# Optimization experiments

Hardware: AMD Instinct MI355X
Metric: run time of the kernel (lower is better)

Reference implementation:

```python
import jax, jax.numpy as jnp
import numpy as np

N_HIDDEN = 512
BATCH = 16
MAX_LEN = 4096


def setup_inputs() -> dict:
    key = jax.random.key(0)
    k1, k2, k3 = jax.random.split(key, 3)
    h = jax.random.normal(k1, (BATCH, N_HIDDEN, MAX_LEN), dtype=jnp.float32)
    # Conv1d weight [out_ch=3*nh, in_ch=nh, kernel=2], fan-in scaled
    W = jax.random.normal(k2, (3 * N_HIDDEN, N_HIDDEN, 2), dtype=jnp.float32) / np.float32(np.sqrt(2.0 * N_HIDDEN))
    b = 0.02 * jax.random.normal(k3, (3 * N_HIDDEN,), dtype=jnp.float32)
    b = b.at[2 * N_HIDDEN:].set(1.0)  # init_gate_bias on the gate third of the bias
    # lengths: grouped (unique_consecutive) and sorted descending, padded into width MAX_LEN
    N = jnp.array([4096] * 4 + [3000] * 4 + [2048] * 4 + [1000] * 4, dtype=jnp.int32)
    return {"h": h, "W": W, "b": b, "N": N}


def _conv_reduce(h, W, b):
    # _reduce: Conv1d(nh -> 3*nh, kernel=2, stride=2) then gated combine (dropout=0).
    B, C, L = h.shape
    Lp = L + (L % 2)
    x = jnp.pad(h, ((0, 0), (0, 0), (0, Lp - L))).reshape(B, C, Lp // 2, 2)
    lrg = jnp.einsum('bclk,ock->bol', x, W) + b[None, :, None]  # [B, 3C, L//2]
    l = lrg[:, :C]
    r = jnp.tanh(lrg[:, C:2 * C])
    g = jax.nn.sigmoid(lrg[:, 2 * C:])
    return l * g + r * (1.0 - g)


def _forward(h, W, b, N):
    B, nh, L = h.shape
    # Nfp2 = largest power of two <= N ; M = 2*(N - Nfp2)
    Nfp2 = (2 ** jnp.floor(jnp.log2(N.astype(jnp.float32)))).astype(N.dtype)
    M = 2 * (N - Nfp2)
    # --- prefix reduce + suffix cat (padded/masked equivalent of _suffix_cat) ---
    # conv is local (k=2, s=2), so reducing the full padded width gives identical
    # values at the kept positions j < M//2.
    red = _conv_reduce(h, W, b)                      # [B, nh, ceil(L/2)]
    red = jnp.pad(red, ((0, 0), (0, 0), (0, L - red.shape[-1])))
    j = jnp.arange(L)
    half = (M // 2)[:, None]                         # [B, 1]
    take_red = j[None, :] < half                     # first M//2 slots <- reduced prefix
    idx = jnp.where(take_red, j[None, :], jnp.minimum(j[None, :] + half, L - 1))
    suf = jnp.take_along_axis(h, jnp.broadcast_to(idx[:, None, :], (B, nh, L)), axis=2)
    cur = jnp.where(take_red[:, None, :], red, suf)  # per-seq length now Nfp2 (power of 2)
    n = Nfp2
    # --- halving tree reduction; freeze sequences that reached length 1 ---
    steps = int(np.floor(np.log2(L)))
    for _ in range(steps):
        red = _conv_reduce(cur, W, b)
        neww = red.shape[-1]
        active = (n > 1)[:, None, None]
        cur = jnp.where(active, red, cur[:, :, :neww])
        n = jnp.where(n > 1, n // 2, n)
    return cur[:, :, 0]  # squeeze(-1) -> [B, nh]


def reference(h, W, b, N):
    return _forward(h, W, b, N)
```

## Files before the change

kernel.cpp:

```cpp
#include <hip/hip_runtime.h>

#define BATCH 16
#define CH 512
#define OC 1536
#define KDIM 1024
#define LMAX 4096
#define WGLOB_SZ 3145728

typedef __attribute__((ext_vector_type(8))) _Float16 h8v;
typedef __attribute__((ext_vector_type(4))) float f4v;

__device__ __forceinline__ int nfp2_of(int n) { return 1 << (31 - __clz(n)); }

__device__ __forceinline__ unsigned short h2u(_Float16 h) {
  union { _Float16 h; unsigned short u; } v; v.h = h; return v.u;
}

__device__ __forceinline__ void layout(const int* __restrict__ Nvec, int b,
                                       size_t& offC0, size_t& offA, size_t& offB,
                                       int& n, int& nfp2, int& half) {
  size_t c0t = 0, at = 0, bt = 0, c0o = 0, ao = 0, bo = 0;
  n = 2; nfp2 = 2; half = 0;
#pragma unroll 1
  for (int i = 0; i < BATCH; ++i) {
    int ni = Nvec[i];
    int f = nfp2_of(ni);
    int hf = ni - f;
    size_t cs = (size_t)((hf + 127) & ~127) << 11;
    size_t as = (size_t)(f >> 1) << 11;
    size_t bs = (size_t)(f >> 2) << 11;
    if (i < b) { c0o += cs; ao += as; bo += bs; }
    if (i == b) { n = ni; nfp2 = f; half = hf; }
    c0t += cs; at += as; bt += bs;
  }
  offC0 = (size_t)WGLOB_SZ + c0o;
  offA = (size_t)WGLOB_SZ + c0t + ao;
  offB = (size_t)WGLOB_SZ + c0t + at + bo;
}

__device__ __forceinline__ void gload16(const void* g, void* l) {
  __builtin_amdgcn_global_load_lds((const __attribute__((address_space(1))) void*)g,
                                   (__attribute__((address_space(3))) void*)l, 16, 0, 0);
}

__global__ __launch_bounds__(256) void prep_w_k(const float* __restrict__ W, char* __restrict__ ws) {
  int idx = blockIdx.x * 256 + threadIdx.x;
  if (idx >= 16 * 1536) return;
  int step = idx / 1536;
  int o = idx - step * 1536;
  const float* src = W + (size_t)o * KDIM + step * 64;
  unsigned short hb[64];
#pragma unroll
  for (int t = 0; t < 64; ++t) hb[t] = h2u((_Float16)src[t]);
  uint4* d4 = (uint4*)(ws + ((size_t)idx << 7));
#pragma unroll
  for (int s = 0; s < 8; ++s) {
    int oc = (s ^ (o & 7)) * 8;
    uint4 v;
    v.x = (unsigned)hb[oc + 0] | ((unsigned)hb[oc + 1] << 16);
    v.y = (unsigned)hb[oc + 2] | ((unsigned)hb[oc + 3] << 16);
    v.z = (unsigned)hb[oc + 4] | ((unsigned)hb[oc + 5] << 16);
    v.w = (unsigned)hb[oc + 6] | ((unsigned)hb[oc + 7] << 16);
    d4[s] = v;
  }
}

__global__ __launch_bounds__(256) void reorg_h_k(const float* __restrict__ h,
                                                 const int* __restrict__ Nvec,
                                                 char* __restrict__ ws,
                                                 float* __restrict__ dout, int mode) {
  __shared__ char T[32 * 256];
  const int b = blockIdx.z;
  size_t offC0, offA, offB; int n, nfp2, half;
  layout(Nvec, b, offC0, offA, offB, n, nfp2, half);
  const int tid = threadIdx.x;
  const int by = blockIdx.y;
  const int c0 = by * 64;

  if (mode == 1 && nfp2 == 1) {
    if (blockIdx.x == 0 && tid < 64)
      dout[(size_t)b * CH + c0 + tid] = h[(size_t)b * CH * LMAX + (size_t)(c0 + tid) * LMAX];
    return;
  }

  const int d0 = blockIdx.x * 32;
  int dlo, dhi, soff;
  size_t base;
  if (mode == 0) { dlo = 0; dhi = half; soff = 0; base = offC0; }
  else { dlo = half >> 1; dhi = nfp2 >> 1; soff = half; base = offA; }
  if (d0 >= dhi || d0 + 32 <= dlo) return;

  const float* hb = h + (size_t)b * CH * LMAX;

#pragma unroll
  for (int q = 0; q < 8; ++q) {
    int id = q * 256 + tid;
    int cl = id >> 5;
    int dl = id & 31;
    int d = d0 + dl;
    bool ok = (d < dhi) && (d >= dlo);
    float2 v;
    v.x = 0.f; v.y = 0.f;
    if (ok) v = *(const float2*)(hb + (size_t)(c0 + cl) * LMAX + 2 * d + soff);
    unsigned u = (unsigned)h2u((_Float16)v.x) | ((unsigned)h2u((_Float16)v.y) << 16);
    int g = cl >> 2;
    *(unsigned*)(T + dl * 256 + ((g ^ (dl & 15)) << 4) + (cl & 3) * 4) = u;
  }
  __syncthreads();
#pragma unroll
  for (int qq = 0; qq < 2; ++qq) {
    int gid = qq * 256 + tid;
    int dl = gid >> 4;
    int s = gid & 15;
    int d = d0 + dl;
    if (d >= dhi || d < dlo) continue;
    uint4 val = *(const uint4*)(T + dl * 256 + ((s ^ (dl & 15)) << 4));
    size_t dst = base + ((size_t)d << 11) + (size_t)((2 * by + (s >> 3)) << 7) +
                 (((s & 7) ^ (d & 7)) << 4);
    *(uint4*)(ws + dst) = val;
  }
}

__global__ __launch_bounds__(256, 2) void mfma_level_k(const float* __restrict__ bias,
                                                       const int* __restrict__ Nvec,
                                                       char* __restrict__ ws,
                                                       float* __restrict__ dout,
                                                       int level, int tiles) {
  __shared__ char smem[81920];
  const int id = blockIdx.x;
  const int o0 = (id & 7) * 64;
  const int r2 = id >> 3;
  const int xb = r2 % tiles;
  const int b = r2 / tiles;
  if (b >= BATCH) return;

  size_t offC0, offA, offB; int n, nfp2, half;
  layout(Nvec, b, offC0, offA, offB, n, nfp2, half);

  int cols;
  size_t inOff, outOff;
  if (level == 0) {
    if (half == 0) return;
    cols = half;
    inOff = offC0;
    outOff = offA;
  } else {
    int w = nfp2 >> (level - 1);
    if (w < 2) return;
    cols = w >> 1;
    inOff = (level & 1) ? offA : offB;
    outOff = (level & 1) ? offB : offA;
  }
  const bool fin = (level > 0) && ((nfp2 >> level) == 1);
  const int l0 = xb * 128;
  if (l0 >= cols) return;

  const int tid = threadIdx.x;
  const int lane = tid & 63, wid = tid >> 6;
  const int lane15 = lane & 15, lq = lane >> 4;
  const int rg = wid & 1, cg = wid >> 1;
  const char* inp = ws + inOff;

  unsigned aoff[6]; int adst[6];
#pragma unroll
  for (int q = 0; q < 6; ++q) {
    int d = q * 4096 + tid * 16;
    int r = d >> 7;
    int p = d & 127;
    int o = ((r >> 6) << 9) + o0 + (r & 63);
    aoff[q] = ((unsigned)o << 7) + p;
    adst[q] = q * 4096 + wid * 1024;
  }
  unsigned boff[4]; int bdst[4];
#pragma unroll
  for (int q = 0; q < 4; ++q) {
    int d = q * 4096 + tid * 16;
    int l = d >> 7;
    int p = d & 127;
    int lc = l0 + l; if (lc > cols - 1) lc = cols - 1;
    boff[q] = ((unsigned)lc << 11) + p;
    bdst[q] = q * 4096 + wid * 1024;
  }

#define STAGE(st, sel) do {                                                  \
    char* Ab = smem + (sel) * 24576;                                         \
    char* Bb = smem + 49152 + (sel) * 16384;                                 \
    unsigned ka = (unsigned)(st) * 196608u;                                  \
    unsigned kb = (unsigned)(st) << 7;                                       \
    _Pragma("unroll") for (int q = 0; q < 6; ++q)                            \
      gload16(ws + ka + aoff[q], Ab + adst[q]);                              \
    _Pragma("unroll") for (int q = 0; q < 4; ++q)                            \
      gload16(inp + kb + boff[q], Bb + bdst[q]);                             \
  } while (0)

  f4v acc[6][4];
#pragma unroll
  for (int m = 0; m < 6; ++m)
#pragma unroll
    for (int cf = 0; cf < 4; ++cf) acc[m][cf] = (f4v){0.f, 0.f, 0.f, 0.f};

  STAGE(0, 0);
  __syncthreads();

#pragma unroll 1
  for (int st = 0; st < 16; ++st) {
    const int cur = st & 1;
    if (st + 1 < 16) STAGE(st + 1, cur ^ 1);
    const char* Asb = smem + cur * 24576;
    const char* Bsb = smem + 49152 + cur * 16384;

#pragma unroll
    for (int s2 = 0; s2 < 2; ++s2) {
      const int oct = (s2 << 2) | lq;
      h8v bh[4];
#pragma unroll
      for (int cf = 0; cf < 4; ++cf) {
        int ll = cg * 64 + cf * 16 + lane15;
        bh[cf] = *(const h8v*)(Bsb + ll * 128 + ((oct ^ (ll & 7)) << 4));
      }
#pragma unroll
      for (int m = 0; m < 6; ++m) {
        int rr = (m >> 1) * 64 + rg * 32 + (m & 1) * 16 + lane15;
        h8v ah = *(const h8v*)(Asb + rr * 128 + ((oct ^ (rr & 7)) << 4));
#pragma unroll
        for (int cf = 0; cf < 4; ++cf)
          acc[m][cf] = __builtin_amdgcn_mfma_f32_16x16x32_f16(ah, bh[cf], acc[m][cf], 0, 0, 0);
      }
    }
    __syncthreads();
  }
#undef STAGE

  char* outp = ws + outOff;
#pragma unroll
  for (int s = 0; s < 2; ++s) {
#pragma unroll
    for (int cf = 0; cf < 4; ++cf) {
      f4v vl = acc[s][cf], vr = acc[2 + s][cf], vg = acc[4 + s][cf];
      int l = l0 + cg * 64 + cf * 16 + lane15;
      if (l >= cols) continue;
      int P = l >> 1, par = l & 1;
#pragma unroll
      for (int j = 0; j < 4; ++j) {
        int c = o0 + rg * 32 + s * 16 + lq * 4 + j;
        float zl = vl[j] + bias[c];
        float zr = vr[j] + bias[CH + c];
        float zg = vg[j] + bias[2 * CH + c];
        float g = 1.f / (1.f + __expf(-zg));
        float rt = 1.f - 2.f / (1.f + __expf(2.f * zr));
        float val = zl * g + rt * (1.f - g);
        if (fin) {
          if (l == 0) dout[(size_t)b * CH + c] = val;
        } else {
          int k = 2 * c + par;
          size_t byte = ((size_t)P << 11) + (size_t)((k >> 6) << 7) +
                        ((((k >> 3) & 7) ^ (P & 7)) << 4) + ((k & 7) << 1);
          *(unsigned short*)(outp + byte) = h2u((_Float16)val);
        }
      }
    }
  }
}

extern "C" void kernel_launch(void* const* d_in, const int* in_sizes, int n_in,
                              void* d_out, int out_size, void* d_ws, size_t ws_size,
                              hipStream_t stream) {
  const float* h = (const float*)d_in[0];
  const float* W = (const float*)d_in[1];
  const float* bias = (const float*)d_in[2];
  const int* Nvec = (const int*)d_in[3];
  float* dout = (float*)d_out;
  char* ws = (char*)d_ws;

  prep_w_k<<<dim3(96), 256, 0, stream>>>(W, ws);
  reorg_h_k<<<dim3(64, 8, BATCH), 256, 0, stream>>>(h, Nvec, ws, dout, 0);
  reorg_h_k<<<dim3(64, 8, BATCH), 256, 0, stream>>>(h, Nvec, ws, dout, 1);

  mfma_level_k<<<dim3(8 * 8 * BATCH), 256, 0, stream>>>(bias, Nvec, ws, dout, 0, 8);
  for (int lev = 1; lev <= 12; ++lev) {
    int colsmax = LMAX >> lev;
    int tiles = (colsmax + 127) / 128; if (tiles < 1) tiles = 1;
    mfma_level_k<<<dim3(tiles * 8 * BATCH), 256, 0, stream>>>(bias, Nvec, ws, dout, lev, tiles);
  }
}
```

Measured before the change: 494.5 us.

## Fuse small tree levels into one persistent kernel with per-batch atomic barriers

```diff
diff --git a/kernel.cpp b/kernel.cpp
--- a/kernel.cpp
+++ b/kernel.cpp
@@ -6,6 +6,7 @@
 #define KDIM 1024
 #define LMAX 4096
 #define WGLOB_SZ 3145728
+#define CTR_OFF 76546048
 
 typedef __attribute__((ext_vector_type(8))) _Float16 h8v;
 typedef __attribute__((ext_vector_type(4))) float f4v;
@@ -42,6 +43,10 @@
   __builtin_amdgcn_global_load_lds((const __attribute__((address_space(1))) void*)g,
                                    (__attribute__((address_space(3))) void*)l, 16, 0, 0);
 }
+__device__ __forceinline__ void gload16c(const void* g, void* l) {
+  __builtin_amdgcn_global_load_lds((const __attribute__((address_space(1))) void*)g,
+                                   (__attribute__((address_space(3))) void*)l, 16, 0, 1);
+}
 
 __global__ __launch_bounds__(256) void prep_w_k(const float* __restrict__ W, char* __restrict__ ws) {
   int idx = blockIdx.x * 256 + threadIdx.x;
@@ -63,6 +68,10 @@
     v.w = (unsigned)hb[oc + 6] | ((unsigned)hb[oc + 7] << 16);
     d4[s] = v;
   }
+}
+
+__global__ void init_ctr_k(char* __restrict__ ws) {
+  ((unsigned*)(ws + CTR_OFF))[threadIdx.x] = 0u;
 }
 
 __global__ __launch_bounds__(256) void reorg_h_k(const float* __restrict__ h,
@@ -121,117 +130,10 @@
   }
 }
 
-__global__ __launch_bounds__(256, 2) void mfma_level_k(const float* __restrict__ bias,
-                                                       const int* __restrict__ Nvec,
-                                                       char* __restrict__ ws,
-                                                       float* __restrict__ dout,
-                                                       int level, int tiles) {
-  __shared__ char smem[81920];
-  const int id = blockIdx.x;
-  const int o0 = (id & 7) * 64;
-  const int r2 = id >> 3;
-  const int xb = r2 % tiles;
-  const int b = r2 / tiles;
-  if (b >= BATCH) return;
-
-  size_t offC0, offA, offB; int n, nfp2, half;
-  layout(Nvec, b, offC0, offA, offB, n, nfp2, half);
-
-  int cols;
-  size_t inOff, outOff;
-  if (level == 0) {
-    if (half == 0) return;
-    cols = half;
-    inOff = offC0;
-    outOff = offA;
-  } else {
-    int w = nfp2 >> (level - 1);
-    if (w < 2) return;
-    cols = w >> 1;
-    inOff = (level & 1) ? offA : offB;
-    outOff = (level & 1) ? offB : offA;
-  }
-  const bool fin = (level > 0) && ((nfp2 >> level) == 1);
-  const int l0 = xb * 128;
-  if (l0 >= cols) return;
-
-  const int tid = threadIdx.x;
-  const int lane = tid & 63, wid = tid >> 6;
-  const int lane15 = lane & 15, lq = lane >> 4;
-  const int rg = wid & 1, cg = wid >> 1;
-  const char* inp = ws + inOff;
-
-  unsigned aoff[6]; int adst[6];
-#pragma unroll
-  for (int q = 0; q < 6; ++q) {
-    int d = q * 4096 + tid * 16;
-    int r = d >> 7;
-    int p = d & 127;
-    int o = ((r >> 6) << 9) + o0 + (r & 63);
-    aoff[q] = ((unsigned)o << 7) + p;
-    adst[q] = q * 4096 + wid * 1024;
-  }
-  unsigned boff[4]; int bdst[4];
-#pragma unroll
-  for (int q = 0; q < 4; ++q) {
-    int d = q * 4096 + tid * 16;
-    int l = d >> 7;
-    int p = d & 127;
-    int lc = l0 + l; if (lc > cols - 1) lc = cols - 1;
-    boff[q] = ((unsigned)lc << 11) + p;
-    bdst[q] = q * 4096 + wid * 1024;
-  }
-
-#define STAGE(st, sel) do {                                                  \
-    char* Ab = smem + (sel) * 24576;                                         \
-    char* Bb = smem + 49152 + (sel) * 16384;                                 \
-    unsigned ka = (unsigned)(st) * 196608u;                                  \
-    unsigned kb = (unsigned)(st) << 7;                                       \
-    _Pragma("unroll") for (int q = 0; q < 6; ++q)                            \
-      gload16(ws + ka + aoff[q], Ab + adst[q]);                              \
-    _Pragma("unroll") for (int q = 0; q < 4; ++q)                            \
-      gload16(inp + kb + boff[q], Bb + bdst[q]);                             \
-  } while (0)
-
-  f4v acc[6][4];
-#pragma unroll
-  for (int m = 0; m < 6; ++m)
-#pragma unroll
-    for (int cf = 0; cf < 4; ++cf) acc[m][cf] = (f4v){0.f, 0.f, 0.f, 0.f};
-
-  STAGE(0, 0);
-  __syncthreads();
-
-#pragma unroll 1
-  for (int st = 0; st < 16; ++st) {
-    const int cur = st & 1;
-    if (st + 1 < 16) STAGE(st + 1, cur ^ 1);
-    const char* Asb = smem + cur * 24576;
-    const char* Bsb = smem + 49152 + cur * 16384;
-
-#pragma unroll
-    for (int s2 = 0; s2 < 2; ++s2) {
-      const int oct = (s2 << 2) | lq;
-      h8v bh[4];
-#pragma unroll
-      for (int cf = 0; cf < 4; ++cf) {
-        int ll = cg * 64 + cf * 16 + lane15;
-        bh[cf] = *(const h8v*)(Bsb + ll * 128 + ((oct ^ (ll & 7)) << 4));
-      }
-#pragma unroll
-      for (int m = 0; m < 6; ++m) {
-        int rr = (m >> 1) * 64 + rg * 32 + (m & 1) * 16 + lane15;
-        h8v ah = *(const h8v*)(Asb + rr * 128 + ((oct ^ (rr & 7)) << 4));
-#pragma unroll
-        for (int cf = 0; cf < 4; ++cf)
-          acc[m][cf] = __builtin_amdgcn_mfma_f32_16x16x32_f16(ah, bh[cf], acc[m][cf], 0, 0, 0);
-      }
-    }
-    __syncthreads();
-  }
-#undef STAGE
-
-  char* outp = ws + outOff;
+__device__ __forceinline__ void gate_store(const f4v acc[6][4], const float* __restrict__ bias,
+                                           char* outp, float* __restrict__ dout,
+                                           int b, int o0, int rg, int cg, int lq, int lane15,
+                                           int l0, int cols, bool fin) {
 #pragma unroll
   for (int s = 0; s < 2; ++s) {
 #pragma unroll
@@ -262,6 +164,236 @@
   }
 }
 
+__global__ __launch_bounds__(256, 2) void mfma_level_k(const float* __restrict__ bias,
+                                                       const int* __restrict__ Nvec,
+                                                       char* __restrict__ ws,
+                                                       float* __restrict__ dout,
+                                                       int level, int tiles) {
+  __shared__ char smem[81920];
+  const int id = blockIdx.x;
+  const int o0 = (id & 7) * 64;
+  const int r2 = id >> 3;
+  const int xb = r2 % tiles;
+  const int b = r2 / tiles;
+  if (b >= BATCH) return;
+
+  size_t offC0, offA, offB; int n, nfp2, half;
+  layout(Nvec, b, offC0, offA, offB, n, nfp2, half);
+
+  int cols;
+  size_t inOff, outOff;
+  if (level == 0) {
+    if (half == 0) return;
+    cols = half;
+    inOff = offC0;
+    outOff = offA;
+  } else {
+    int w = nfp2 >> (level - 1);
+    if (w < 2) return;
+    cols = w >> 1;
+    if (cols <= 128) return;
+    inOff = (level & 1) ? offA : offB;
+    outOff = (level & 1) ? offB : offA;
+  }
+  const int l0 = xb * 128;
+  if (l0 >= cols) return;
+
+  const int tid = threadIdx.x;
+  const int lane = tid & 63, wid = tid >> 6;
+  const int lane15 = lane & 15, lq = lane >> 4;
+  const int rg = wid & 1, cg = wid >> 1;
+  const char* inp = ws + inOff;
+
+  unsigned aoff[6]; int adst[6];
+#pragma unroll
+  for (int q = 0; q < 6; ++q) {
+    int d = q * 4096 + tid * 16;
+    int r = d >> 7;
+    int p = d & 127;
+    int o = ((r >> 6) << 9) + o0 + (r & 63);
+    aoff[q] = ((unsigned)o << 7) + p;
+    adst[q] = q * 4096 + wid * 1024;
+  }
+  unsigned boff[4]; int bdst[4];
+#pragma unroll
+  for (int q = 0; q < 4; ++q) {
+    int d = q * 4096 + tid * 16;
+    int l = d >> 7;
+    int p = d & 127;
+    int lc = l0 + l; if (lc > cols - 1) lc = cols - 1;
+    boff[q] = ((unsigned)lc << 11) + p;
+    bdst[q] = q * 4096 + wid * 1024;
+  }
+
+#define STAGE(st, sel) do {                                                  \
+    char* Ab = smem + (sel) * 24576;                                         \
+    char* Bb = smem + 49152 + (sel) * 16384;                                 \
+    unsigned ka = (unsigned)(st) * 196608u;                                  \
+    unsigned kb = (unsigned)(st) << 7;                                       \
+    _Pragma("unroll") for (int q = 0; q < 6; ++q)                            \
+      gload16(ws + ka + aoff[q], Ab + adst[q]);                              \
+    _Pragma("unroll") for (int q = 0; q < 4; ++q)                            \
+      gload16(inp + kb + boff[q], Bb + bdst[q]);                             \
+  } while (0)
+
+  f4v acc[6][4];
+#pragma unroll
+  for (int m = 0; m < 6; ++m)
+#pragma unroll
+    for (int cf = 0; cf < 4; ++cf) acc[m][cf] = (f4v){0.f, 0.f, 0.f, 0.f};
+
+  STAGE(0, 0);
+  __syncthreads();
+
+#pragma unroll 1
+  for (int st = 0; st < 16; ++st) {
+    const int cur = st & 1;
+    if (st + 1 < 16) STAGE(st + 1, cur ^ 1);
+    const char* Asb = smem + cur * 24576;
+    const char* Bsb = smem + 49152 + cur * 16384;
+
+#pragma unroll
+    for (int s2 = 0; s2 < 2; ++s2) {
+      const int oct = (s2 << 2) | lq;
+      h8v bh[4];
+#pragma unroll
+      for (int cf = 0; cf < 4; ++cf) {
+        int ll = cg * 64 + cf * 16 + lane15;
+        bh[cf] = *(const h8v*)(Bsb + ll * 128 + ((oct ^ (ll & 7)) << 4));
+      }
+#pragma unroll
+      for (int m = 0; m < 6; ++m) {
+        int rr = (m >> 1) * 64 + rg * 32 + (m & 1) * 16 + lane15;
+        h8v ah = *(const h8v*)(Asb + rr * 128 + ((oct ^ (rr & 7)) << 4));
+#pragma unroll
+        for (int cf = 0; cf < 4; ++cf)
+          acc[m][cf] = __builtin_amdgcn_mfma_f32_16x16x32_f16(ah, bh[cf], acc[m][cf], 0, 0, 0);
+      }
+    }
+    __syncthreads();
+  }
+#undef STAGE
+
+  bool fin = (level > 0) && ((nfp2 >> level) == 1);
+  gate_store(acc, bias, ws + outOff, dout, b, o0, rg, cg, lq, lane15, l0, cols, fin);
+}
+
+__global__ __launch_bounds__(256, 2) void tail_k(const float* __restrict__ bias,
+                                                 const int* __restrict__ Nvec,
+                                                 char* __restrict__ ws,
+                                                 float* __restrict__ dout) {
+  __shared__ char smem[81920];
+  const int id = blockIdx.x;
+  const int b = id & 15;
+  const int o0 = (id >> 4) * 64;
+
+  size_t offC0, offA, offB; int n, nfp2, half;
+  layout(Nvec, b, offC0, offA, offB, n, nfp2, half);
+  if (nfp2 < 2) return;
+
+  const int tid = threadIdx.x;
+  const int lane = tid & 63, wid = tid >> 6;
+  const int lane15 = lane & 15, lq = lane >> 4;
+  const int rg = wid & 1, cg = wid >> 1;
+
+  unsigned aoff[6]; int adst[6];
+#pragma unroll
+  for (int q = 0; q < 6; ++q) {
+    int d = q * 4096 + tid * 16;
+    int r = d >> 7;
+    int p = d & 127;
+    int o = ((r >> 6) << 9) + o0 + (r & 63);
+    aoff[q] = ((unsigned)o << 7) + p;
+    adst[q] = q * 4096 + wid * 1024;
+  }
+
+  unsigned* ctr = (unsigned*)(ws + CTR_OFF) + b * 16;
+
+  int lev = 1;
+  while ((nfp2 >> lev) > 128) ++lev;
+
+#pragma unroll 1
+  for (;; ++lev) {
+    int w = nfp2 >> (lev - 1);
+    if (w < 2) break;
+    const int cols = nfp2 >> lev;
+    const bool fin = (cols == 1);
+    const char* inp = ws + ((lev & 1) ? offA : offB);
+    char* outp = ws + ((lev & 1) ? offB : offA);
+
+    unsigned boff[4]; int bdst[4];
+#pragma unroll
+    for (int q = 0; q < 4; ++q) {
+      int d = q * 4096 + tid * 16;
+      int l = d >> 7;
+      int p = d & 127;
+      int lc = l; if (lc > cols - 1) lc = cols - 1;
+      boff[q] = ((unsigned)lc << 11) + p;
+      bdst[q] = q * 4096 + wid * 1024;
+    }
+
+#define STAGE_T(st, sel) do {                                                \
+    char* Ab = smem + (sel) * 24576;                                         \
+    char* Bb = smem + 49152 + (sel) * 16384;                                 \
+    unsigned ka = (unsigned)(st) * 196608u;                                  \
+    unsigned kb = (unsigned)(st) << 7;                                       \
+    _Pragma("unroll") for (int q = 0; q < 6; ++q)                            \
+      gload16(ws + ka + aoff[q], Ab + adst[q]);                              \
+    _Pragma("unroll") for (int q = 0; q < 4; ++q)                            \
+      gload16c(inp + kb + boff[q], Bb + bdst[q]);                            \
+  } while (0)
+
+    f4v acc[6][4];
+#pragma unroll
+    for (int m = 0; m < 6; ++m)
+#pragma unroll
+      for (int cf = 0; cf < 4; ++cf) acc[m][cf] = (f4v){0.f, 0.f, 0.f, 0.f};
+
+    STAGE_T(0, 0);
+    __syncthreads();
+
+#pragma unroll 1
+    for (int st = 0; st < 16; ++st) {
+      const int cur = st & 1;
+      if (st + 1 < 16) STAGE_T(st + 1, cur ^ 1);
+      const char* Asb = smem + cur * 24576;
+      const char* Bsb = smem + 49152 + cur * 16384;
+
+#pragma unroll
+      for (int s2 = 0; s2 < 2; ++s2) {
+        const int oct = (s2 << 2) | lq;
+        h8v bh[4];
+#pragma unroll
+        for (int cf = 0; cf < 4; ++cf) {
+          int ll = cg * 64 + cf * 16 + lane15;
+          bh[cf] = *(const h8v*)(Bsb + ll * 128 + ((oct ^ (ll & 7)) << 4));
+        }
+#pragma unroll
+        for (int m = 0; m < 6; ++m) {
+          int rr = (m >> 1) * 64 + rg * 32 + (m & 1) * 16 + lane15;
+          h8v ah = *(const h8v*)(Asb + rr * 128 + ((oct ^ (rr & 7)) << 4));
+#pragma unroll
+          for (int cf = 0; cf < 4; ++cf)
+            acc[m][cf] = __builtin_amdgcn_mfma_f32_16x16x32_f16(ah, bh[cf], acc[m][cf], 0, 0, 0);
+        }
+      }
+      __syncthreads();
+    }
+#undef STAGE_T
+
+    gate_store(acc, bias, outp, dout, b, o0, rg, cg, lq, lane15, 0, cols, fin);
+    if (fin) break;
+
+    __threadfence();
+    __syncthreads();
+    if (tid == 0) {
+      atomicAdd(ctr + lev, 1u);
+      while (atomicAdd(ctr + lev, 0u) < 8u) __builtin_amdgcn_s_sleep(8);
+    }
+    __syncthreads();
+  }
+}
+
 extern "C" void kernel_launch(void* const* d_in, const int* in_sizes, int n_in,
                               void* d_out, int out_size, void* d_ws, size_t ws_size,
                               hipStream_t stream) {
@@ -273,13 +405,14 @@
   char* ws = (char*)d_ws;
 
   prep_w_k<<<dim3(96), 256, 0, stream>>>(W, ws);
+  init_ctr_k<<<dim3(1), 256, 0, stream>>>(ws);
   reorg_h_k<<<dim3(64, 8, BATCH), 256, 0, stream>>>(h, Nvec, ws, dout, 0);
   reorg_h_k<<<dim3(64, 8, BATCH), 256, 0, stream>>>(h, Nvec, ws, dout, 1);
 
   mfma_level_k<<<dim3(8 * 8 * BATCH), 256, 0, stream>>>(bias, Nvec, ws, dout, 0, 8);
-  for (int lev = 1; lev <= 12; ++lev) {
-    int colsmax = LMAX >> lev;
-    int tiles = (colsmax + 127) / 128; if (tiles < 1) tiles = 1;
+  for (int lev = 1; lev <= 4; ++lev) {
+    int tiles = (LMAX >> lev) / 128;
     mfma_level_k<<<dim3(tiles * 8 * BATCH), 256, 0, stream>>>(bias, Nvec, ws, dout, lev, tiles);
   }
-}
+  tail_k<<<dim3(128), 256, 0, stream>>>(bias, Nvec, ws, dout);
+}
```

Measured after the change: 527.3 us. 6.6% more time.
